# Kernel optimization log

Measured on AMD Instinct MI355X. Metric: run time of the kernel, lower is better.

The kernel has to match this reference:

```python
import jax, jax.numpy as jnp
import numpy as np

SCALE = 0.125  # 1/sqrt(D=64)

def setup_inputs() -> dict:
    key = jax.random.key(0)
    k1, k2 = jax.random.split(key)
    x1 = jax.random.normal(k1, (16, 2048, 64), dtype=jnp.float32)
    x2 = jax.random.normal(k2, (16, 2048, 64), dtype=jnp.float32)
    return {"x1": x1, "x2": x2}

def reference(x1, x2):
    # scores: [B, Sq, Sk]
    scores = jnp.einsum('bqd,bkd->bqk', x1, x2) * SCALE
    attn = jax.nn.softmax(scores, axis=-1)
    # dropout_p=0 (eval): identity
    out = jnp.einsum('bqk,bkd->bqd', attn, x2)
    return out
```

## Files before the change

### kernel.cpp

```cpp
#include <hip/hip_runtime.h>
#include <hip/hip_bf16.h>

typedef __attribute__((ext_vector_type(8))) short bf16x8;
typedef __attribute__((ext_vector_type(16))) float f32x16;

__device__ __forceinline__ unsigned short f2b(float f) {
  __hip_bfloat16 h = __float2bfloat16(f);
  unsigned short u; __builtin_memcpy(&u, &h, sizeof(u));
  return u;
}
__device__ __forceinline__ unsigned int pk2(float lo, float hi) {
  unsigned int r;
  asm("v_cvt_pk_bf16_f32 %0, %1, %2" : "=v"(r) : "v"(lo), "v"(hi));
  return r;
}
__device__ __forceinline__ float vexp2(float x) {
  float r; asm("v_exp_f32 %0, %1" : "=v"(r) : "v"(x)); return r;
}
__device__ __forceinline__ float fcomp(const float4& v, int i) {
  return i == 0 ? v.x : i == 1 ? v.y : i == 2 ? v.z : v.w;
}

constexpr int S_LEN = 2048;
constexpr int DIM   = 64;
constexpr float SC_LOG2E = 0.125f * 1.44269504088896f;
constexpr float MC_LOG2  = 6.0f * 1.44269504088896f;
constexpr float THR_RAW  = 8.0f / SC_LOG2E;

__global__ __launch_bounds__(256)
void prep_kv(const float* __restrict__ x2, unsigned char* __restrict__ img) {
  __shared__ unsigned short Kst[64][80];
  const int blk = blockIdx.x;
  const int s   = threadIdx.x;
  const float* src   = x2 + (size_t)blk * 4096;
  unsigned char* dst = img + (size_t)blk * 16384;
  {
    int row = s >> 2, c16 = (s & 3) * 16;
    const float* p = src + row * 64 + c16;
    float4 a0 = *reinterpret_cast<const float4*>(p + 0);
    float4 a1 = *reinterpret_cast<const float4*>(p + 4);
    float4 a2 = *reinterpret_cast<const float4*>(p + 8);
    float4 a3 = *reinterpret_cast<const float4*>(p + 12);
    uint4 u0, u1;
    u0.x = pk2(a0.x, a0.y); u0.y = pk2(a0.z, a0.w);
    u0.z = pk2(a1.x, a1.y); u0.w = pk2(a1.z, a1.w);
    u1.x = pk2(a2.x, a2.y); u1.y = pk2(a2.z, a2.w);
    u1.z = pk2(a3.x, a3.y); u1.w = pk2(a3.z, a3.w);
    *reinterpret_cast<uint4*>(&Kst[row][c16 + 0]) = u0;
    *reinterpret_cast<uint4*>(&Kst[row][c16 + 8]) = u1;
  }
  __syncthreads();
  #pragma unroll
  for (int half = 0; half < 2; ++half) {
    int c = s + half * 256;
    int f = c >> 6, l = c & 63;
    int kt = f >> 2, cc = f & 3, rr = l & 31, hh = l >> 5;
    uint4 u = *reinterpret_cast<const uint4*>(&Kst[kt * 32 + rr][cc * 16 + hh * 8]);
    *reinterpret_cast<uint4*>(dst + f * 1024 + l * 16) = u;
  }
  #pragma unroll
  for (int half = 0; half < 2; ++half) {
    int c = s + half * 256;
    int g = c >> 6, l = c & 63;
    int dt = g & 1, kc = (g >> 1) & 1, kt = g >> 2;
    int rr = l & 31, hh = l >> 5;
    int d = dt * 32 + rr, k0 = kt * 32 + kc * 16 + hh * 8;
    unsigned int wv[4];
    #pragma unroll
    for (int jj = 0; jj < 4; ++jj)
      wv[jj] = (unsigned int)Kst[k0 + 2 * jj][d] |
               ((unsigned int)Kst[k0 + 2 * jj + 1][d] << 16);
    uint4 u; u.x = wv[0]; u.y = wv[1]; u.z = wv[2]; u.w = wv[3];
    *reinterpret_cast<uint4*>(dst + 8192 + g * 1024 + l * 16) = u;
  }
}

__device__ __forceinline__ void ld4(bf16x8 (&d)[4], const unsigned char* p) {
  d[0] = *reinterpret_cast<const bf16x8*>(p);
  d[1] = *reinterpret_cast<const bf16x8*>(p + 1024);
  d[2] = *reinterpret_cast<const bf16x8*>(p + 2048);
  d[3] = *reinterpret_cast<const bf16x8*>(p + 3072);
}

__device__ __forceinline__ void qk2(const bf16x8 (&k)[4], const bf16x8 (&q0)[4],
                                    const bf16x8 (&q1)[4], f32x16& s0, f32x16& s1) {
  #pragma unroll
  for (int i = 0; i < 16; ++i) { s0[i] = 0.f; s1[i] = 0.f; }
  __builtin_amdgcn_s_setprio(1);
  #pragma unroll
  for (int c = 0; c < 4; ++c) {
    s0 = __builtin_amdgcn_mfma_f32_32x32x16_bf16(k[c], q0[c], s0, 0, 0, 0);
    s1 = __builtin_amdgcn_mfma_f32_32x32x16_bf16(k[c], q1[c], s1, 0, 0, 0);
  }
  __builtin_amdgcn_s_setprio(0);
}

__device__ __forceinline__ void exppv(f32x16& st, const bf16x8 (&vf)[4],
                                      f32x16 (&oacc)[2], float (&ps)[8]) {
  #pragma unroll
  for (int i = 0; i < 16; ++i) st[i] = vexp2(fmaf(st[i], SC_LOG2E, -MC_LOG2));
  #pragma unroll
  for (int i = 0; i < 8; ++i) ps[i] += st[i] + st[i + 8];
  unsigned int own[8];
  #pragma unroll
  for (int a = 0; a < 4; ++a) {
    own[a * 2 + 0] = pk2(st[4 * a + 0], st[4 * a + 1]);
    own[a * 2 + 1] = pk2(st[4 * a + 2], st[4 * a + 3]);
  }
  __builtin_amdgcn_s_setprio(1);
  #pragma unroll
  for (int kc = 0; kc < 2; ++kc) {
    unsigned int p0 = own[4 * kc + 0], p2 = own[4 * kc + 2];
    unsigned int p1 = own[4 * kc + 1], p3 = own[4 * kc + 3];
    asm("v_permlane32_swap_b32 %0, %1" : "+v"(p0), "+v"(p2));
    asm("v_permlane32_swap_b32 %0, %1" : "+v"(p1), "+v"(p3));
    union { unsigned int u[4]; bf16x8 v; } pf;
    pf.u[0] = p0; pf.u[1] = p1; pf.u[2] = p2; pf.u[3] = p3;
    oacc[0] = __builtin_amdgcn_mfma_f32_32x32x16_bf16(vf[kc * 2 + 0], pf.v, oacc[0], 0, 0, 0);
    oacc[1] = __builtin_amdgcn_mfma_f32_32x32x16_bf16(vf[kc * 2 + 1], pf.v, oacc[1], 0, 0, 0);
  }
  __builtin_amdgcn_s_setprio(0);
}

__global__ __launch_bounds__(256, 2)
void attn_fwd5(const float* __restrict__ x1, const unsigned char* __restrict__ img,
               float* __restrict__ out) {
  __shared__ float Ocmb[4 * 64 * 68 + 4 * 64];

  const int logical = (blockIdx.x & 7) * 64 + (blockIdx.x >> 3);
  const int b   = logical >> 5;
  const int qg  = logical & 31;
  const int tid = threadIdx.x;
  const int kh  = tid >> 6;
  const int lane = tid & 63, r = lane & 31, hi = lane >> 5;

  const float* Qp = x1 + ((size_t)b * S_LEN + qg * 64 + r) * DIM;
  bf16x8 qf0[4], qf1[4];
  #pragma unroll
  for (int c = 0; c < 4; ++c) {
    const float* p0 = Qp + 16 * c + 8 * hi;
    const float* p1 = p0 + 32 * DIM;
    bf16x8 v0, v1;
    #pragma unroll
    for (int j = 0; j < 8; ++j) { v0[j] = (short)f2b(p0[j]); v1[j] = (short)f2b(p1[j]); }
    qf0[c] = v0; qf1[c] = v1;
  }

  f32x16 oacc0[2], oacc1[2];
  #pragma unroll
  for (int i = 0; i < 16; ++i) {
    oacc0[0][i] = 0.f; oacc0[1][i] = 0.f;
    oacc1[0][i] = 0.f; oacc1[1][i] = 0.f;
  }
  float ps0[8], ps1[8];
  #pragma unroll
  for (int i = 0; i < 8; ++i) { ps0[i] = 0.f; ps1[i] = 0.f; }

  const unsigned char* tb = img + ((size_t)(b * 32 + kh * 8)) * 16384 + lane * 16;

  bf16x8 kA[4], vA[4];
  f32x16 sA0, sA1, sB0, sB1;

  ld4(kA, tb);
  qk2(kA, qf0, qf1, sA0, sA1);
  ld4(kA, tb + 4096);
  ld4(vA, tb + 8192);

  #pragma unroll 1
  for (int t = 0; t < 8; ++t) {
    const unsigned char* base  = tb + (size_t)t * 16384;
    const unsigned char* nbase = tb + (size_t)(t < 7 ? t + 1 : t) * 16384;

    qk2(kA, qf0, qf1, sB0, sB1);
    ld4(kA, nbase);
    exppv(sA0, vA, oacc0, ps0);
    exppv(sA1, vA, oacc1, ps1);
    ld4(vA, base + 8192 + 4096);

    qk2(kA, qf0, qf1, sA0, sA1);
    ld4(kA, nbase + 4096);
    exppv(sB0, vA, oacc0, ps0);
    exppv(sB1, vA, oacc1, ps1);
    ld4(vA, nbase + 8192);
  }

  #pragma unroll
  for (int s2 = 4; s2 > 0; s2 >>= 1)
    #pragma unroll
    for (int i = 0; i < s2; ++i) { ps0[i] += ps0[i + s2]; ps1[i] += ps1[i + s2]; }
  float l0 = ps0[0] + __shfl_xor(ps0[0], 32);
  float l1 = ps1[0] + __shfl_xor(ps1[0], 32);

  float* Oc = Ocmb;
  float* lb = Ocmb + 4 * 64 * 68;
  #pragma unroll
  for (int dt = 0; dt < 2; ++dt)
    #pragma unroll
    for (int i = 0; i < 16; ++i) {
      int d = dt * 32 + (i & 3) + 8 * (i >> 2) + 4 * hi;
      Oc[(kh * 64 + r) * 68 + d]      = oacc0[dt][i];
      Oc[(kh * 64 + 32 + r) * 68 + d] = oacc1[dt][i];
    }
  if (hi == 0) {
    lb[kh * 64 + r]      = l0;
    lb[kh * 64 + 32 + r] = l1;
  }
  __syncthreads();

  const int q  = tid >> 2;
  const int sg = (tid & 3) * 16;
  float l = lb[0 * 64 + q] + lb[1 * 64 + q] + lb[2 * 64 + q] + lb[3 * 64 + q];
  float inv = 1.0f / l;
  float* dst = out + ((size_t)b * S_LEN + qg * 64 + q) * DIM + sg;
  #pragma unroll
  for (int j4 = 0; j4 < 4; ++j4) {
    float4 o;
    o.x = (Oc[(0 * 64 + q) * 68 + sg + j4 * 4 + 0] + Oc[(1 * 64 + q) * 68 + sg + j4 * 4 + 0] +
           Oc[(2 * 64 + q) * 68 + sg + j4 * 4 + 0] + Oc[(3 * 64 + q) * 68 + sg + j4 * 4 + 0]) * inv;
    o.y = (Oc[(0 * 64 + q) * 68 + sg + j4 * 4 + 1] + Oc[(1 * 64 + q) * 68 + sg + j4 * 4 + 1] +
           Oc[(2 * 64 + q) * 68 + sg + j4 * 4 + 1] + Oc[(3 * 64 + q) * 68 + sg + j4 * 4 + 1]) * inv;
    o.z = (Oc[(0 * 64 + q) * 68 + sg + j4 * 4 + 2] + Oc[(1 * 64 + q) * 68 + sg + j4 * 4 + 2] +
           Oc[(2 * 64 + q) * 68 + sg + j4 * 4 + 2] + Oc[(3 * 64 + q) * 68 + sg + j4 * 4 + 2]) * inv;
    o.w = (Oc[(0 * 64 + q) * 68 + sg + j4 * 4 + 3] + Oc[(1 * 64 + q) * 68 + sg + j4 * 4 + 3] +
           Oc[(2 * 64 + q) * 68 + sg + j4 * 4 + 3] + Oc[(3 * 64 + q) * 68 + sg + j4 * 4 + 3]) * inv;
    *reinterpret_cast<float4*>(dst + j4 * 4) = o;
  }
}

__device__ __forceinline__ void compute_tile_fb(const unsigned char* Kb, const unsigned char* Vb,
                                                const bf16x8 (&qf)[4], f32x16 (&oacc)[2],
                                                float& m_run, float& lsum,
                                                int r, int hi, int kkey, int vkey) {
  f32x16 st[2];
  #pragma unroll
  for (int kt = 0; kt < 2; ++kt) {
    f32x16 acc;
    #pragma unroll
    for (int i = 0; i < 16; ++i) acc[i] = 0.f;
    #pragma unroll
    for (int c = 0; c < 4; ++c) {
      bf16x8 a = *reinterpret_cast<const bf16x8*>(
          Kb + (kt * 32 + r) * 128 + ((32 * c + 16 * hi) ^ kkey));
      acc = __builtin_amdgcn_mfma_f32_32x32x16_bf16(a, qf[c], acc, 0, 0, 0);
    }
    st[kt] = acc;
  }
  float mt[16];
  #pragma unroll
  for (int i = 0; i < 16; ++i) mt[i] = fmaxf(st[0][i], st[1][i]);
  #pragma unroll
  for (int sfs = 8; sfs > 0; sfs >>= 1)
    #pragma unroll
    for (int i = 0; i < sfs; ++i) mt[i] = fmaxf(mt[i], mt[i + sfs]);
  float mx = fmaxf(mt[0], __shfl_xor(mt[0], 32));
  if (!__all(mx <= m_run + THR_RAW)) {
    float mnew  = fmaxf(m_run, mx);
    float alpha = exp2f((m_run - mnew) * SC_LOG2E);
    m_run = mnew; lsum *= alpha;
    #pragma unroll
    for (int i = 0; i < 16; ++i) { oacc[0][i] *= alpha; oacc[1][i] *= alpha; }
  }
  float mc = m_run * SC_LOG2E;
  float pt[16];
  #pragma unroll
  for (int kt = 0; kt < 2; ++kt)
    #pragma unroll
    for (int i = 0; i < 16; ++i)
      st[kt][i] = vexp2(fmaf(st[kt][i], SC_LOG2E, -mc));
  #pragma unroll
  for (int i = 0; i < 16; ++i) pt[i] = st[0][i] + st[1][i];
  #pragma unroll
  for (int sfs = 8; sfs > 0; sfs >>= 1)
    #pragma unroll
    for (int i = 0; i < sfs; ++i) pt[i] += pt[i + sfs];
  lsum += pt[0] + __shfl_xor(pt[0], 32);
  #pragma unroll
  for (int kt = 0; kt < 2; ++kt) {
    unsigned int own[8], cross[8];
    #pragma unroll
    for (int a = 0; a < 4; ++a) {
      own[a * 2 + 0] = pk2(st[kt][4 * a + 0], st[kt][4 * a + 1]);
      own[a * 2 + 1] = pk2(st[kt][4 * a + 2], st[kt][4 * a + 3]);
    }
    #pragma unroll
    for (int e = 0; e < 8; ++e) cross[e] = __shfl_xor(own[e], 32);
    #pragma unroll
    for (int kc = 0; kc < 2; ++kc) {
      union { unsigned int u[4]; bf16x8 v; } pf;
      pf.u[0] = hi ? cross[4 * kc + 2] : own[4 * kc + 0];
      pf.u[1] = hi ? cross[4 * kc + 3] : own[4 * kc + 1];
      pf.u[2] = hi ? own[4 * kc + 2]   : cross[4 * kc + 0];
      pf.u[3] = hi ? own[4 * kc + 3]   : cross[4 * kc + 1];
      #pragma unroll
      for (int dt = 0; dt < 2; ++dt) {
        bf16x8 vf = *reinterpret_cast<const bf16x8*>(
            Vb + (dt * 32 + r) * 128 + ((64 * kt + 32 * kc + 16 * hi) ^ vkey));
        oacc[dt] = __builtin_amdgcn_mfma_f32_32x32x16_bf16(vf, pf.v, oacc[dt], 0, 0, 0);
      }
    }
  }
}

__global__ __launch_bounds__(512, 4)
void attn_mono(const float* __restrict__ x1, const float* __restrict__ x2,
               float* __restrict__ out) {
  __shared__ __align__(16) unsigned char smem[69632];
  __shared__ float mlbuf[4][2][64];
  const int logical = (blockIdx.x & 7) * 64 + (blockIdx.x >> 3);
  const int b = logical >> 5, q0 = (logical & 31) * 64;
  const int tid = threadIdx.x, wave = tid >> 6, pair = wave >> 1, wid = wave & 1;
  const int lane = tid & 63, r = lane & 31, hi = lane >> 5, tp = tid & 127;
  const int kkey = (r & 7) << 4, vkey = ((r >> 2) & 7) << 4;
  unsigned char* Kb = smem + pair * 16384;
  unsigned char* Vb = Kb + 8192;
  const float* Qp = x1 + ((size_t)b * S_LEN + q0 + wid * 32 + r) * DIM;
  bf16x8 qf[4];
  #pragma unroll
  for (int c = 0; c < 4; ++c) {
    const float* p = Qp + 16 * c + 8 * hi;
    bf16x8 v;
    #pragma unroll
    for (int j = 0; j < 8; ++j) v[j] = (short)f2b(p[j]);
    qf[c] = v;
  }
  f32x16 oacc[2];
  #pragma unroll
  for (int i = 0; i < 16; ++i) { oacc[0][i] = 0.f; oacc[1][i] = 0.f; }
  float m_run = -3.0e38f, lsum = 0.f;
  #pragma unroll 1
  for (int t = 0; t < 8; ++t) {
    __syncthreads();
    const float* src = x2 + ((size_t)b * S_LEN + (size_t)(pair * 8 + t) * 64) * DIM;
    #pragma unroll
    for (int sb = 0; sb < 2; ++sb) {
      int s = tp + sb * 128;
      int rowg = s >> 4, colg = s & 15;
      const float* p = src + 4 * rowg * DIM + 4 * colg;
      float4 w0 = *reinterpret_cast<const float4*>(p + 0 * DIM);
      float4 w1 = *reinterpret_cast<const float4*>(p + 1 * DIM);
      float4 w2 = *reinterpret_cast<const float4*>(p + 2 * DIM);
      float4 w3 = *reinterpret_cast<const float4*>(p + 3 * DIM);
      #pragma unroll
      for (int i = 0; i < 4; ++i) {
        int row = 4 * rowg + i;
        float4 wv = i == 0 ? w0 : i == 1 ? w1 : i == 2 ? w2 : w3;
        uint2 u; u.x = pk2(wv.x, wv.y); u.y = pk2(wv.z, wv.w);
        *reinterpret_cast<uint2*>(Kb + row * 128 + ((8 * colg) ^ ((row & 7) << 4))) = u;
      }
      int vkeyw = (colg & 7) << 4;
      #pragma unroll
      for (int i = 0; i < 4; ++i) {
        int d = 4 * colg + i;
        uint2 u;
        u.x = pk2(fcomp(w0, i), fcomp(w1, i));
        u.y = pk2(fcomp(w2, i), fcomp(w3, i));
        *reinterpret_cast<uint2*>(Vb + d * 128 + ((8 * rowg) ^ vkeyw)) = u;
      }
    }
    __syncthreads();
    compute_tile_fb(Kb, Vb, qf, oacc, m_run, lsum, r, hi, kkey, vkey);
  }
  __syncthreads();
  if (hi == 0) {
    mlbuf[pair][0][wid * 32 + r] = m_run;
    mlbuf[pair][1][wid * 32 + r] = lsum;
  }
  float* Ocomb = reinterpret_cast<float*>(smem);
  #pragma unroll
  for (int dt = 0; dt < 2; ++dt)
    #pragma unroll
    for (int i = 0; i < 16; ++i) {
      int d = dt * 32 + (i & 3) + 8 * (i >> 2) + 4 * hi;
      Ocomb[(pair * 64 + wid * 32 + r) * 67 + d] = oacc[dt][i];
    }
  __syncthreads();
  int q = tid >> 3, dg = tid & 7;
  float m0 = mlbuf[0][0][q], m1 = mlbuf[1][0][q], m2 = mlbuf[2][0][q], m3 = mlbuf[3][0][q];
  float l0 = mlbuf[0][1][q], l1 = mlbuf[1][1][q], l2 = mlbuf[2][1][q], l3 = mlbuf[3][1][q];
  float msx = fmaxf(fmaxf(m0, m1), fmaxf(m2, m3));
  float w0 = exp2f((m0 - msx) * SC_LOG2E);
  float w1 = exp2f((m1 - msx) * SC_LOG2E);
  float w2 = exp2f((m2 - msx) * SC_LOG2E);
  float w3 = exp2f((m3 - msx) * SC_LOG2E);
  float inv = 1.0f / (l0 * w0 + l1 * w1 + l2 * w2 + l3 * w3);
  float o[8];
  #pragma unroll
  for (int j = 0; j < 8; ++j)
    o[j] = (Ocomb[(0 * 64 + q) * 67 + dg * 8 + j] * w0 +
            Ocomb[(1 * 64 + q) * 67 + dg * 8 + j] * w1 +
            Ocomb[(2 * 64 + q) * 67 + dg * 8 + j] * w2 +
            Ocomb[(3 * 64 + q) * 67 + dg * 8 + j] * w3) * inv;
  float* outp = out + ((size_t)b * S_LEN + q0 + q) * DIM + dg * 8;
  float4 s0; s0.x = o[0]; s0.y = o[1]; s0.z = o[2]; s0.w = o[3];
  float4 s1; s1.x = o[4]; s1.y = o[5]; s1.z = o[6]; s1.w = o[7];
  *reinterpret_cast<float4*>(outp + 0) = s0;
  *reinterpret_cast<float4*>(outp + 4) = s1;
}

extern "C" void kernel_launch(void* const* d_in, const int* in_sizes, int n_in,
                              void* d_out, int out_size, void* d_ws, size_t ws_size,
                              hipStream_t stream) {
  const float* x1 = (const float*)d_in[0];
  const float* x2 = (const float*)d_in[1];
  float* outp = (float*)d_out;
  const size_t need = (size_t)512 * 16384;
  if (ws_size >= need) {
    prep_kv<<<dim3(512), dim3(256), 0, stream>>>(x2, (unsigned char*)d_ws);
    attn_fwd5<<<dim3(512), dim3(256), 0, stream>>>(x1, (const unsigned char*)d_ws, outp);
  } else {
    attn_mono<<<dim3(512), dim3(512), 0, stream>>>(x1, x2, outp);
  }
}
```

Before: 37.72 us.

## Software-pipeline attention loop: split exp/pack from PV MFMA with sched barriers

Restructures the main K/V loop into a deeper software pipeline. The exp and bf16 pack of one score tile now happens a stage earlier, separate from its PV MFMAs, and sched_barrier fences stop the compiler from reordering the stages. The aim is to overlap the VALU exp work with MFMA and memory loads, and the PV MFMAs for both query halves are batched. It also changes the block-to-logical mapping to interleave batch/query groups and shortens the row-sum reduction. Risks are higher register pressure from the extra PF buffers and whether the hand-imposed schedule beats the compiler's.

Measured after the change: 39.50 us. +4.7%, slower.

```diff
diff --git a/kernel.cpp b/kernel.cpp
--- a/kernel.cpp
+++ b/kernel.cpp
@@ -75,6 +75,8 @@
   }
 }
 
+struct PF { uint4 a, b; };
+
 __device__ __forceinline__ void ld4(bf16x8 (&d)[4], const unsigned char* p) {
   d[0] = *reinterpret_cast<const bf16x8*>(p);
   d[1] = *reinterpret_cast<const bf16x8*>(p + 1024);
@@ -95,39 +97,66 @@
   __builtin_amdgcn_s_setprio(0);
 }
 
-__device__ __forceinline__ void exppv(f32x16& st, const bf16x8 (&vf)[4],
-                                      f32x16 (&oacc)[2], float (&ps)[8]) {
+__device__ __forceinline__ void exppack(f32x16& st, float (&ps)[4], PF& pf) {
   #pragma unroll
   for (int i = 0; i < 16; ++i) st[i] = vexp2(fmaf(st[i], SC_LOG2E, -MC_LOG2));
   #pragma unroll
-  for (int i = 0; i < 8; ++i) ps[i] += st[i] + st[i + 8];
+  for (int i = 0; i < 4; ++i)
+    ps[i] += (st[i] + st[i + 4]) + (st[i + 8] + st[i + 12]);
   unsigned int own[8];
   #pragma unroll
   for (int a = 0; a < 4; ++a) {
     own[a * 2 + 0] = pk2(st[4 * a + 0], st[4 * a + 1]);
     own[a * 2 + 1] = pk2(st[4 * a + 2], st[4 * a + 3]);
   }
-  __builtin_amdgcn_s_setprio(1);
-  #pragma unroll
-  for (int kc = 0; kc < 2; ++kc) {
-    unsigned int p0 = own[4 * kc + 0], p2 = own[4 * kc + 2];
-    unsigned int p1 = own[4 * kc + 1], p3 = own[4 * kc + 3];
+  {
+    unsigned int p0 = own[0], p2 = own[2], p1 = own[1], p3 = own[3];
     asm("v_permlane32_swap_b32 %0, %1" : "+v"(p0), "+v"(p2));
     asm("v_permlane32_swap_b32 %0, %1" : "+v"(p1), "+v"(p3));
-    union { unsigned int u[4]; bf16x8 v; } pf;
-    pf.u[0] = p0; pf.u[1] = p1; pf.u[2] = p2; pf.u[3] = p3;
-    oacc[0] = __builtin_amdgcn_mfma_f32_32x32x16_bf16(vf[kc * 2 + 0], pf.v, oacc[0], 0, 0, 0);
-    oacc[1] = __builtin_amdgcn_mfma_f32_32x32x16_bf16(vf[kc * 2 + 1], pf.v, oacc[1], 0, 0, 0);
-  }
+    pf.a.x = p0; pf.a.y = p1; pf.a.z = p2; pf.a.w = p3;
+  }
+  {
+    unsigned int p0 = own[4], p2 = own[6], p1 = own[5], p3 = own[7];
+    asm("v_permlane32_swap_b32 %0, %1" : "+v"(p0), "+v"(p2));
+    asm("v_permlane32_swap_b32 %0, %1" : "+v"(p1), "+v"(p3));
+    pf.b.x = p0; pf.b.y = p1; pf.b.z = p2; pf.b.w = p3;
+  }
+}
+
+__device__ __forceinline__ bf16x8 u4b(const uint4& u) {
+  bf16x8 v; __builtin_memcpy(&v, &u, 16); return v;
+}
+
+__device__ __forceinline__ void pv(const PF& pf0, const PF& pf1, const bf16x8 (&vf)[4],
+                                   f32x16 (&o0)[2], f32x16 (&o1)[2]) {
+  __builtin_amdgcn_s_setprio(1);
+  o0[0] = __builtin_amdgcn_mfma_f32_32x32x16_bf16(vf[0], u4b(pf0.a), o0[0], 0, 0, 0);
+  o0[1] = __builtin_amdgcn_mfma_f32_32x32x16_bf16(vf[1], u4b(pf0.a), o0[1], 0, 0, 0);
+  o1[0] = __builtin_amdgcn_mfma_f32_32x32x16_bf16(vf[0], u4b(pf1.a), o1[0], 0, 0, 0);
+  o1[1] = __builtin_amdgcn_mfma_f32_32x32x16_bf16(vf[1], u4b(pf1.a), o1[1], 0, 0, 0);
+  o0[0] = __builtin_amdgcn_mfma_f32_32x32x16_bf16(vf[2], u4b(pf0.b), o0[0], 0, 0, 0);
+  o0[1] = __builtin_amdgcn_mfma_f32_32x32x16_bf16(vf[3], u4b(pf0.b), o0[1], 0, 0, 0);
+  o1[0] = __builtin_amdgcn_mfma_f32_32x32x16_bf16(vf[2], u4b(pf1.b), o1[0], 0, 0, 0);
+  o1[1] = __builtin_amdgcn_mfma_f32_32x32x16_bf16(vf[3], u4b(pf1.b), o1[1], 0, 0, 0);
   __builtin_amdgcn_s_setprio(0);
 }
 
+__device__ __forceinline__ const unsigned char* kaddr(const unsigned char* tb, int p) {
+  int pc = p < 15 ? p : 15;
+  return tb + (size_t)(pc >> 1) * 16384 + (pc & 1) * 4096;
+}
+__device__ __forceinline__ const unsigned char* vaddr(const unsigned char* tb, int p) {
+  int pc = p < 15 ? p : 15;
+  return tb + (size_t)(pc >> 1) * 16384 + 8192 + (pc & 1) * 4096;
+}
+
 __global__ __launch_bounds__(256, 2)
-void attn_fwd5(const float* __restrict__ x1, const unsigned char* __restrict__ img,
+void attn_fwd6(const float* __restrict__ x1, const unsigned char* __restrict__ img,
                float* __restrict__ out) {
   __shared__ float Ocmb[4 * 64 * 68 + 4 * 64];
 
-  const int logical = (blockIdx.x & 7) * 64 + (blockIdx.x >> 3);
+  const int bid = blockIdx.x;
+  const int logical = (bid & 7) * 64 + ((bid >> 3) & 31) * 2 + (bid >> 8);
   const int b   = logical >> 5;
   const int qg  = logical & 31;
   const int tid = threadIdx.x;
@@ -152,44 +181,51 @@
     oacc0[0][i] = 0.f; oacc0[1][i] = 0.f;
     oacc1[0][i] = 0.f; oacc1[1][i] = 0.f;
   }
-  float ps0[8], ps1[8];
-  #pragma unroll
-  for (int i = 0; i < 8; ++i) { ps0[i] = 0.f; ps1[i] = 0.f; }
+  float ps0[4], ps1[4];
+  #pragma unroll
+  for (int i = 0; i < 4; ++i) { ps0[i] = 0.f; ps1[i] = 0.f; }
 
   const unsigned char* tb = img + ((size_t)(b * 32 + kh * 8)) * 16384 + lane * 16;
 
   bf16x8 kA[4], vA[4];
   f32x16 sA0, sA1, sB0, sB1;
-
-  ld4(kA, tb);
+  PF pA0, pA1, pB0, pB1;
+
+  ld4(kA, kaddr(tb, 0));
   qk2(kA, qf0, qf1, sA0, sA1);
-  ld4(kA, tb + 4096);
-  ld4(vA, tb + 8192);
+  ld4(kA, kaddr(tb, 1));
+  ld4(vA, vaddr(tb, 0));
+  __builtin_amdgcn_sched_barrier(0);
+  qk2(kA, qf0, qf1, sB0, sB1);
+  ld4(kA, kaddr(tb, 2));
+  __builtin_amdgcn_sched_barrier(0);
+  exppack(sA0, ps0, pA0); exppack(sA1, ps1, pA1);
 
   #pragma unroll 1
-  for (int t = 0; t < 8; ++t) {
-    const unsigned char* base  = tb + (size_t)t * 16384;
-    const unsigned char* nbase = tb + (size_t)(t < 7 ? t + 1 : t) * 16384;
-
+  for (int p = 0; p < 16; p += 2) {
+    pv(pA0, pA1, vA, oacc0, oacc1);
+    ld4(vA, vaddr(tb, p + 1));
+    __builtin_amdgcn_sched_barrier(0);
+    qk2(kA, qf0, qf1, sA0, sA1);
+    ld4(kA, kaddr(tb, p + 3));
+    __builtin_amdgcn_sched_barrier(0);
+    exppack(sB0, ps0, pB0); exppack(sB1, ps1, pB1);
+
+    pv(pB0, pB1, vA, oacc0, oacc1);
+    ld4(vA, vaddr(tb, p + 2));
+    __builtin_amdgcn_sched_barrier(0);
     qk2(kA, qf0, qf1, sB0, sB1);
-    ld4(kA, nbase);
-    exppv(sA0, vA, oacc0, ps0);
-    exppv(sA1, vA, oacc1, ps1);
-    ld4(vA, base + 8192 + 4096);
-
-    qk2(kA, qf0, qf1, sA0, sA1);
-    ld4(kA, nbase + 4096);
-    exppv(sB0, vA, oacc0, ps0);
-    exppv(sB1, vA, oacc1, ps1);
-    ld4(vA, nbase + 8192);
-  }
-
-  #pragma unroll
-  for (int s2 = 4; s2 > 0; s2 >>= 1)
-    #pragma unroll
-    for (int i = 0; i < s2; ++i) { ps0[i] += ps0[i + s2]; ps1[i] += ps1[i + s2]; }
-  float l0 = ps0[0] + __shfl_xor(ps0[0], 32);
-  float l1 = ps1[0] + __shfl_xor(ps1[0], 32);
+    ld4(kA, kaddr(tb, p + 4));
+    __builtin_amdgcn_sched_barrier(0);
+    if (p < 14) {
+      exppack(sA0, ps0, pA0); exppack(sA1, ps1, pA1);
+    }
+  }
+
+  float l0 = (ps0[0] + ps0[1]) + (ps0[2] + ps0[3]);
+  float l1 = (ps1[0] + ps1[1]) + (ps1[2] + ps1[3]);
+  l0 += __shfl_xor(l0, 32);
+  l1 += __shfl_xor(l1, 32);
 
   float* Oc = Ocmb;
   float* lb = Ocmb + 4 * 64 * 68;
@@ -406,7 +442,7 @@
   const size_t need = (size_t)512 * 16384;
   if (ws_size >= need) {
     prep_kv<<<dim3(512), dim3(256), 0, stream>>>(x2, (unsigned char*)d_ws);
-    attn_fwd5<<<dim3(512), dim3(256), 0, stream>>>(x1, (const unsigned char*)d_ws, outp);
+    attn_fwd6<<<dim3(512), dim3(256), 0, stream>>>(x1, (const unsigned char*)d_ws, outp);
   } else {
     attn_mono<<<dim3(512), dim3(512), 0, stream>>>(x1, x2, outp);
   }
```
